# Optimization experiments

Hardware: AMD Instinct MI355X
Metric: run time of the kernel (lower is better)

## Reference

```python
import jax, jax.numpy as jnp
import numpy as np

H = 4          # num_heads
D = 32         # out_dim per head (P, A, state all 32)
NP_ = 30000    # number of P nodes
NA_ = 30000    # number of A nodes
NS_ = 1        # single global state node
E = 400000     # edges per agent-agent edge type
ALPHA = 0.2    # leaky-relu negative slope


def _edge_type(Wh_et, Wh_dst, a_src, a_dst, src, dst, n_dst):
    """GAT attention + edge-softmax + scatter-aggregate for one edge type.
    Wh_et: [N_src,H,D] edge-type projected src features; Wh_dst: [N_dst,H,D]."""
    es = jnp.sum(Wh_et * a_src, axis=-1)    # [N_src,H]
    ed = jnp.sum(Wh_dst * a_dst, axis=-1)   # [N_dst,H]
    e = es[src] + ed[dst]                   # [E,H] u_add_v
    e = jnp.where(e > 0, e, ALPHA * e)      # leaky relu
    m = jax.ops.segment_max(e, dst, num_segments=n_dst)
    m = jnp.where(jnp.isfinite(m), m, 0.0)  # guard empty segments
    w = jnp.exp(e - m[dst])                 # [E,H]
    denom = jax.ops.segment_sum(w, dst, num_segments=n_dst)
    a = w / denom[dst]                      # edge softmax over dst neighborhoods
    msg = Wh_et[src] * a[:, :, None]        # [E,H,D] u_mul_e
    return jax.ops.segment_sum(msg, dst, num_segments=n_dst)  # fn.sum


def setup_inputs() -> dict:
    key = jax.random.key(0)
    ks = iter(jax.random.split(key, 64))
    nrm = lambda shape, s=0.05: jax.random.normal(next(ks), shape, jnp.float32) * s
    inp = {}
    inp['feat_P'] = nrm((NP_, 128), 1.0)
    inp['feat_A'] = nrm((NA_, 128), 1.0)
    inp['feat_state'] = nrm((NS_, 64), 1.0)
    for name, din in [('P', 128), ('A', 128), ('p2p', 128), ('p2a', 128),
                      ('a2p', 128), ('a2a', 128), ('p2s', 128), ('a2s', 128), ('in', 64)]:
        inp['W_' + name] = nrm((din, H * D))
        inp['b_' + name] = nrm((H * D,))
    for et in ['p2p', 'p2a', 'a2p', 'a2a', 'p2s', 'a2s']:
        inp['attn_%s_src' % et] = nrm((H, D))
        inp['attn_%s_dst' % et] = nrm((H, D))
    ri = lambda n, hi: jax.random.randint(next(ks), (n,), 0, hi, jnp.int32)
    inp['src_p2p'] = ri(E, NP_); inp['dst_p2p'] = ri(E, NP_)
    inp['src_p2a'] = ri(E, NP_); inp['dst_p2a'] = ri(E, NA_)
    inp['src_a2p'] = ri(E, NA_); inp['dst_a2p'] = ri(E, NP_)
    inp['src_a2a'] = ri(E, NA_); inp['dst_a2a'] = ri(E, NA_)
    inp['src_p2s'] = jnp.arange(NP_, dtype=jnp.int32); inp['dst_p2s'] = jnp.zeros((NP_,), jnp.int32)
    inp['src_a2s'] = jnp.arange(NA_, dtype=jnp.int32); inp['dst_a2s'] = jnp.zeros((NA_,), jnp.int32)
    return inp


def reference(feat_P, feat_A, feat_state,
              W_P, b_P, W_A, b_A, W_p2p, b_p2p, W_p2a, b_p2a, W_a2p, b_a2p,
              W_a2a, b_a2a, W_p2s, b_p2s, W_a2s, b_a2s, W_in, b_in,
              attn_p2p_src, attn_p2p_dst, attn_p2a_src, attn_p2a_dst,
              attn_a2p_src, attn_a2p_dst, attn_a2a_src, attn_a2a_dst,
              attn_p2s_src, attn_p2s_dst, attn_a2s_src, attn_a2s_dst,
              src_p2p, dst_p2p, src_p2a, dst_p2a, src_a2p, dst_a2p,
              src_a2a, dst_a2a, src_p2s, dst_p2s, src_a2s, dst_a2s):
    lin = lambda x, W, b: (x @ W + b).reshape(-1, H, D)
    # self transforms
    Wh_P = lin(feat_P, W_P, b_P)
    Wh_A = lin(feat_A, W_A, b_A)
    Wh_in = lin(feat_state, W_in, b_in)
    # per-edge-type transforms
    Wh_p2p = lin(feat_P, W_p2p, b_p2p)
    Wh_p2a = lin(feat_P, W_p2a, b_p2a)
    Wh_a2p = lin(feat_A, W_a2p, b_a2p)
    Wh_a2a = lin(feat_A, W_a2a, b_a2a)
    Wh_p2s = lin(feat_P, W_p2s, b_p2s)
    Wh_a2s = lin(feat_A, W_a2s, b_a2s)
    # attention + edge softmax + aggregate per edge type
    ft_p2p = _edge_type(Wh_p2p, Wh_P, attn_p2p_src, attn_p2p_dst, src_p2p, dst_p2p, NP_)
    ft_a2p = _edge_type(Wh_a2p, Wh_P, attn_a2p_src, attn_a2p_dst, src_a2p, dst_a2p, NP_)
    ft_p2a = _edge_type(Wh_p2a, Wh_A, attn_p2a_src, attn_p2a_dst, src_p2a, dst_p2a, NA_)
    ft_a2a = _edge_type(Wh_a2a, Wh_A, attn_a2a_src, attn_a2a_dst, src_a2a, dst_a2a, NA_)
    ft_p2s = _edge_type(Wh_p2s, Wh_in, attn_p2s_src, attn_p2s_dst, src_p2s, dst_p2s, NS_)
    ft_a2s = _edge_type(Wh_a2s, Wh_in, attn_a2s_src, attn_a2s_dst, src_a2s, dst_a2s, NS_)
    out_P = jax.nn.relu(Wh_P + ft_p2p + ft_a2p)      # [NP,H,D]
    out_A = jax.nn.relu(Wh_A + ft_p2a + ft_a2a)      # [NA,H,D]
    out_S = jax.nn.relu(Wh_in + ft_p2s + ft_a2s)     # [1,H,D]
    # concat along node axis (all out dims are D) for a single output tensor
    return jnp.concatenate([out_P, out_A, out_S], axis=0)
```

## Files before the change

### kernel.cpp

```cpp
#include <hip/hip_runtime.h>

#define NP 30000
#define NA 30000
#define EDG 400000
#define HD 128
#define LRELU_ALPHA 0.2f
#define NODE_STRIDE 30016
#define TILE 32
#define BPJ 938

__device__ __forceinline__ float lrelu(float x) { return x > 0.f ? x : LRELU_ALPHA * x; }

struct GJob {
    const float* A; const float* W; const float* bias;
    float* C;
    const float* a1; float* o1;
    const float* a2; float* o2;
    int mode;
};
struct GJobs { GJob j[4]; };

__launch_bounds__(256)
__global__ void gemm_multi(GJobs js)
{
    const GJob J = js.j[blockIdx.y];
    __shared__ float As[TILE * 128];
    __shared__ float red[4][128];
    __shared__ float dred[4][4];
    const int t = threadIdx.x;
    const int row0 = blockIdx.x * TILE;
    const int M = NP;
    #pragma unroll
    for (int i = 0; i < 4; ++i) {
        int f4 = t + i * 256;
        int r = f4 >> 5, c4 = f4 & 31;
        int gr = row0 + r;
        float4 v = make_float4(0.f, 0.f, 0.f, 0.f);
        if (gr < M) v = reinterpret_cast<const float4*>(J.A)[(size_t)gr * 32 + c4];
        reinterpret_cast<float4*>(As)[f4] = v;
    }
    __syncthreads();
    const int cg = t & 63;
    const int rg = t >> 6;
    float acc0[8], acc1[8];
    #pragma unroll
    for (int r = 0; r < 8; ++r) { acc0[r] = 0.f; acc1[r] = 0.f; }
    const float* Asr = &As[rg * 8 * 128];
    const float* W = J.W;
    for (int k = 0; k < 128; k += 4) {
        float w00 = W[(k+0)*128 + cg],    w01 = W[(k+1)*128 + cg],
              w02 = W[(k+2)*128 + cg],    w03 = W[(k+3)*128 + cg];
        float w10 = W[(k+0)*128 + cg+64], w11 = W[(k+1)*128 + cg+64],
              w12 = W[(k+2)*128 + cg+64], w13 = W[(k+3)*128 + cg+64];
        #pragma unroll
        for (int r = 0; r < 8; ++r) {
            float4 f = *reinterpret_cast<const float4*>(&Asr[r * 128 + k]);
            acc0[r] += f.x*w00 + f.y*w01 + f.z*w02 + f.w*w03;
            acc1[r] += f.x*w10 + f.y*w11 + f.z*w12 + f.w*w13;
        }
    }
    float b0 = J.bias[cg], b1 = J.bias[cg + 64];
    #pragma unroll
    for (int r = 0; r < 8; ++r) { acc0[r] += b0; acc1[r] += b1; }

    if (J.mode != 2) {
        #pragma unroll
        for (int r = 0; r < 8; ++r) {
            int gr = row0 + rg * 8 + r;
            if (gr < M) {
                J.C[(size_t)gr * 128 + cg]      = acc0[r];
                J.C[(size_t)gr * 128 + cg + 64] = acc1[r];
            }
        }
        const int nrd = (J.mode == 0) ? 2 : 1;
        float a10 = J.a1[cg], a11 = J.a1[cg + 64];
        float a20 = 0.f, a21 = 0.f;
        if (nrd == 2) { a20 = J.a2[cg]; a21 = J.a2[cg + 64]; }
        #pragma unroll
        for (int r = 0; r < 8; ++r) {
            int node = row0 + rg * 8 + r;
            if (node >= M) break;
            float t10 = acc0[r] * a10, t11 = acc1[r] * a11;
            float t20 = acc0[r] * a20, t21 = acc1[r] * a21;
            #pragma unroll
            for (int off = 16; off; off >>= 1) {
                t10 += __shfl_xor(t10, off, 32);
                t11 += __shfl_xor(t11, off, 32);
                t20 += __shfl_xor(t20, off, 32);
                t21 += __shfl_xor(t21, off, 32);
            }
            if (cg == 0)  { J.o1[node*4+0] = t10; J.o1[node*4+2] = t11;
                            if (nrd == 2) { J.o2[node*4+0] = t20; J.o2[node*4+2] = t21; } }
            if (cg == 32) { J.o1[node*4+1] = t10; J.o1[node*4+3] = t11;
                            if (nrd == 2) { J.o2[node*4+1] = t20; J.o2[node*4+3] = t21; } }
        }
    } else {
        float av0 = J.a1[cg], av1 = J.a1[cg + 64];
        float e0 = J.a2[cg >> 5];
        float e1 = J.a2[2 + (cg >> 5)];
        float sacc0 = 0.f, sacc1 = 0.f, ds0 = 0.f, ds1 = 0.f;
        #pragma unroll
        for (int r = 0; r < 8; ++r) {
            int node = row0 + rg * 8 + r;
            if (node >= M) break;
            float f0 = acc0[r], f1 = acc1[r];
            float t0 = f0 * av0, t1 = f1 * av1;
            #pragma unroll
            for (int off = 16; off; off >>= 1) {
                t0 += __shfl_xor(t0, off, 32);
                t1 += __shfl_xor(t1, off, 32);
            }
            float w0 = __expf(lrelu(t0 + e0));
            float w1 = __expf(lrelu(t1 + e1));
            sacc0 += w0 * f0; sacc1 += w1 * f1;
            ds0 += w0; ds1 += w1;
        }
        red[rg][cg] = sacc0;
        red[rg][cg + 64] = sacc1;
        if (cg == 0)  { dred[rg][0] = ds0; dred[rg][2] = ds1; }
        if (cg == 32) { dred[rg][1] = ds0; dred[rg][3] = ds1; }
        __syncthreads();
        if (t < 128) {
            float s = red[0][t] + red[1][t] + red[2][t] + red[3][t];
            atomicAdd(&J.o1[t], s);
        }
        if (t < 4) {
            float s = dred[0][t] + dred[1][t] + dred[2][t] + dred[3][t];
            atomicAdd(&J.o2[t], s);
        }
    }
}

__global__ void state_lin(const float* __restrict__ feat, const float* __restrict__ W,
                          const float* __restrict__ b, float* __restrict__ out, int K)
{
    int n = threadIdx.x;
    float acc = b[n];
    for (int k = 0; k < K; ++k) acc += feat[k] * W[k * 128 + n];
    out[n] = acc;
}

__global__ void edot2(const float* __restrict__ Wh_inb, const float* __restrict__ aP,
                      const float* __restrict__ aA, float* __restrict__ edsP,
                      float* __restrict__ edsA)
{
    int t = threadIdx.x;
    int l = t & 31;
    float v = Wh_inb[t];
    float p = v * aP[t];
    float q = v * aA[t];
    #pragma unroll
    for (int off = 16; off; off >>= 1) {
        p += __shfl_xor(p, off, 32);
        q += __shfl_xor(q, off, 32);
    }
    if (l == 0) { edsP[t >> 5] = p; edsA[t >> 5] = q; }
}

struct EdgeJobs { const int* src[4]; const int* dst[4]; int* srcsOut[4]; };

__launch_bounds__(256)
__global__ void hist4(EdgeJobs ej, int* __restrict__ counts)
{
    int y = blockIdx.y;
    int e = blockIdx.x * 256 + threadIdx.x;
    if (e < EDG) atomicAdd(&counts[y * NODE_STRIDE + ej.dst[y][e]], 1);
}

__launch_bounds__(1024)
__global__ void scan4(const int* __restrict__ counts, int* __restrict__ offsets,
                      int* __restrict__ cursor, int n)
{
    const int* cnt = counts + blockIdx.x * NODE_STRIDE;
    int* off = offsets + blockIdx.x * NODE_STRIDE;
    int* cur = cursor + blockIdx.x * NODE_STRIDE;
    int t = threadIdx.x;
    int lane = t & 63, wv = t >> 6;
    __shared__ int wsum[16];
    __shared__ int carry_s;
    if (t == 0) { carry_s = 0; off[0] = 0; }
    __syncthreads();
    for (int base = 0; base < n; base += 1024) {
        int i = base + t;
        int v = (i < n) ? cnt[i] : 0;
        int x = v;
        #pragma unroll
        for (int o = 1; o < 64; o <<= 1) {
            int y = __shfl_up(x, o, 64);
            if (lane >= o) x += y;
        }
        if (lane == 63) wsum[wv] = x;
        __syncthreads();
        if (wv == 0) {
            int y = (lane < 16) ? wsum[lane] : 0;
            #pragma unroll
            for (int o = 1; o < 16; o <<= 1) {
                int z = __shfl_up(y, o, 64);
                if (lane >= o) y += z;
            }
            if (lane < 16) wsum[lane] = y;
        }
        __syncthreads();
        int add = carry_s + (wv > 0 ? wsum[wv - 1] : 0);
        int incl = x + add;
        if (i < n) { off[i + 1] = incl; cur[i] = incl - v; }
        __syncthreads();
        if (t == 0) carry_s += wsum[15];
        __syncthreads();
    }
}

__launch_bounds__(256)
__global__ void scatter4(EdgeJobs ej, int* __restrict__ cursor)
{
    int y = blockIdx.y;
    int e = blockIdx.x * 256 + threadIdx.x;
    if (e >= EDG) return;
    int d = ej.dst[y][e];
    int pos = atomicAdd(&cursor[y * NODE_STRIDE + d], 1);
    ej.srcsOut[y][pos] = ej.src[y][e];
}

__launch_bounds__(256)
__global__ void aggregate2(const float* __restrict__ Wh0, const int* __restrict__ off0,
                           const int* __restrict__ srcs0, const float* __restrict__ es0,
                           const float* __restrict__ ed0,
                           const float* __restrict__ Wh1, const int* __restrict__ off1,
                           const int* __restrict__ srcs1, const float* __restrict__ es1,
                           const float* __restrict__ ed1,
                           float* __restrict__ out, int n)
{
    int lane = threadIdx.x & 63;
    int node = (blockIdx.x * blockDim.x + threadIdx.x) >> 6;
    if (node >= n) return;
    const int h = lane >> 4;
    float accX0 = 0.f, accY0 = 0.f, d0 = 0.f;
    float accX1 = 0.f, accY1 = 0.f, d1 = 0.f;
    {
        float edv = ed0[node * 4 + h];
        int b = off0[node], e = off0[node + 1];
        int i = b;
        for (; i + 4 <= e; i += 4) {
            int s0 = srcs0[i], s1 = srcs0[i+1], s2 = srcs0[i+2], s3 = srcs0[i+3];
            float w0 = __expf(lrelu(es0[s0*4 + h] + edv));
            float w1 = __expf(lrelu(es0[s1*4 + h] + edv));
            float w2 = __expf(lrelu(es0[s2*4 + h] + edv));
            float w3 = __expf(lrelu(es0[s3*4 + h] + edv));
            float2 x0 = *reinterpret_cast<const float2*>(&Wh0[(size_t)s0*128 + lane*2]);
            float2 x1 = *reinterpret_cast<const float2*>(&Wh0[(size_t)s1*128 + lane*2]);
            float2 x2 = *reinterpret_cast<const float2*>(&Wh0[(size_t)s2*128 + lane*2]);
            float2 x3 = *reinterpret_cast<const float2*>(&Wh0[(size_t)s3*128 + lane*2]);
            accX0 += w0*x0.x + w1*x1.x + w2*x2.x + w3*x3.x;
            accY0 += w0*x0.y + w1*x1.y + w2*x2.y + w3*x3.y;
            d0 += w0 + w1 + w2 + w3;
        }
        for (; i < e; ++i) {
            int s = srcs0[i];
            float w = __expf(lrelu(es0[s*4 + h] + edv));
            float2 x = *reinterpret_cast<const float2*>(&Wh0[(size_t)s*128 + lane*2]);
            accX0 += w * x.x; accY0 += w * x.y; d0 += w;
        }
    }
    {
        float edv = ed1[node * 4 + h];
        int b = off1[node], e = off1[node + 1];
        int i = b;
        for (; i + 4 <= e; i += 4) {
            int s0 = srcs1[i], s1 = srcs1[i+1], s2 = srcs1[i+2], s3 = srcs1[i+3];
            float w0 = __expf(lrelu(es1[s0*4 + h] + edv));
            float w1 = __expf(lrelu(es1[s1*4 + h] + edv));
            float w2 = __expf(lrelu(es1[s2*4 + h] + edv));
            float w3 = __expf(lrelu(es1[s3*4 + h] + edv));
            float2 x0 = *reinterpret_cast<const float2*>(&Wh1[(size_t)s0*128 + lane*2]);
            float2 x1 = *reinterpret_cast<const float2*>(&Wh1[(size_t)s1*128 + lane*2]);
            float2 x2 = *reinterpret_cast<const float2*>(&Wh1[(size_t)s2*128 + lane*2]);
            float2 x3 = *reinterpret_cast<const float2*>(&Wh1[(size_t)s3*128 + lane*2]);
            accX1 += w0*x0.x + w1*x1.x + w2*x2.x + w3*x3.x;
            accY1 += w0*x0.y + w1*x1.y + w2*x2.y + w3*x3.y;
            d1 += w0 + w1 + w2 + w3;
        }
        for (; i < e; ++i) {
            int s = srcs1[i];
            float w = __expf(lrelu(es1[s*4 + h] + edv));
            float2 x = *reinterpret_cast<const float2*>(&Wh1[(size_t)s*128 + lane*2]);
            accX1 += w * x.x; accY1 += w * x.y; d1 += w;
        }
    }
    float i0 = d0 > 0.f ? 1.f / d0 : 0.f;
    float i1 = d1 > 0.f ? 1.f / d1 : 0.f;
    float2* op = reinterpret_cast<float2*>(out + (size_t)node * 128) + lane;
    float2 o = *op;
    o.x += accX0 * i0 + accX1 * i1;
    o.y += accY0 * i0 + accY1 * i1;
    o.x = o.x > 0.f ? o.x : 0.f;
    o.y = o.y > 0.f ? o.y : 0.f;
    *op = o;
}

__global__ void finalize_state(const float* __restrict__ Wh_in, const float* __restrict__ SS0,
                               const float* __restrict__ dS0, const float* __restrict__ SS1,
                               const float* __restrict__ dS1, float* __restrict__ out)
{
    int t = threadIdx.x;
    int h = t >> 5;
    float v0 = dS0[h]; float i0 = v0 > 0.f ? 1.f / v0 : 0.f;
    float v1 = dS1[h]; float i1 = v1 > 0.f ? 1.f / v1 : 0.f;
    float v = Wh_in[t] + SS0[t] * i0 + SS1[t] * i1;
    out[t] = v > 0.f ? v : 0.f;
}

extern "C" void kernel_launch(void* const* d_in, const int* in_sizes, int n_in,
                              void* d_out, int out_size, void* d_ws, size_t ws_size,
                              hipStream_t stream)
{
    const float* feat_P = (const float*)d_in[0];
    const float* feat_A = (const float*)d_in[1];
    const float* feat_state = (const float*)d_in[2];
    const float* W_P   = (const float*)d_in[3];  const float* b_P   = (const float*)d_in[4];
    const float* W_A   = (const float*)d_in[5];  const float* b_A   = (const float*)d_in[6];
    const float* W_p2p = (const float*)d_in[7];  const float* b_p2p = (const float*)d_in[8];
    const float* W_p2a = (const float*)d_in[9];  const float* b_p2a = (const float*)d_in[10];
    const float* W_a2p = (const float*)d_in[11]; const float* b_a2p = (const float*)d_in[12];
    const float* W_a2a = (const float*)d_in[13]; const float* b_a2a = (const float*)d_in[14];
    const float* W_p2s = (const float*)d_in[15]; const float* b_p2s = (const float*)d_in[16];
    const float* W_a2s = (const float*)d_in[17]; const float* b_a2s = (const float*)d_in[18];
    const float* W_in  = (const float*)d_in[19]; const float* b_in  = (const float*)d_in[20];
    const float* at_p2p_s = (const float*)d_in[21]; const float* at_p2p_d = (const float*)d_in[22];
    const float* at_p2a_s = (const float*)d_in[23]; const float* at_p2a_d = (const float*)d_in[24];
    const float* at_a2p_s = (const float*)d_in[25]; const float* at_a2p_d = (const float*)d_in[26];
    const float* at_a2a_s = (const float*)d_in[27]; const float* at_a2a_d = (const float*)d_in[28];
    const float* at_p2s_s = (const float*)d_in[29]; const float* at_p2s_d = (const float*)d_in[30];
    const float* at_a2s_s = (const float*)d_in[31]; const float* at_a2s_d = (const float*)d_in[32];
    const int* src_p2p = (const int*)d_in[33]; const int* dst_p2p = (const int*)d_in[34];
    const int* src_p2a = (const int*)d_in[35]; const int* dst_p2a = (const int*)d_in[36];
    const int* src_a2p = (const int*)d_in[37]; const int* dst_a2p = (const int*)d_in[38];
    const int* src_a2a = (const int*)d_in[39]; const int* dst_a2a = (const int*)d_in[40];
    float* out = (float*)d_out;

    char* base = (char*)d_ws;
    float* WhT0   = (float*)base;  base += (size_t)NP * HD * 4;
    float* WhT1   = (float*)base;  base += (size_t)NP * HD * 4;
    int* srcs_p2p = (int*)base;    base += (size_t)EDG * 4;
    int* srcs_a2p = (int*)base;    base += (size_t)EDG * 4;
    int* srcs_p2a = (int*)base;    base += (size_t)EDG * 4;
    int* srcs_a2a = (int*)base;    base += (size_t)EDG * 4;
    float* es_p2p = (float*)base;  base += NP * 4 * 4;
    float* es_a2p = (float*)base;  base += NA * 4 * 4;
    float* es_p2a = (float*)base;  base += NP * 4 * 4;
    float* es_a2a = (float*)base;  base += NA * 4 * 4;
    float* ed_p2p = (float*)base;  base += NP * 4 * 4;
    float* ed_a2p = (float*)base;  base += NP * 4 * 4;
    float* ed_p2a = (float*)base;  base += NA * 4 * 4;
    float* ed_a2a = (float*)base;  base += NA * 4 * 4;
    int*   counts = (int*)base;    base += 4 * NODE_STRIDE * 4;
    int*   cursor = (int*)base;    base += 4 * NODE_STRIDE * 4;
    int*   offs   = (int*)base;    base += 4 * NODE_STRIDE * 4;
    float* Wh_inb = (float*)base;  base += 128 * 4;
    float* SS0    = (float*)base;  base += 128 * 4;
    float* SS1    = (float*)base;  base += 128 * 4;
    float* dS0    = (float*)base;  base += 4 * 4;
    float* dS1    = (float*)base;  base += 4 * 4;
    float* edsP   = (float*)base;  base += 4 * 4;
    float* edsA   = (float*)base;  base += 4 * 4;
    size_t needed = (size_t)(base - (char*)d_ws);
    if (ws_size < needed) return;

    int* off_p2p = offs;
    int* off_a2p = offs + NODE_STRIDE;
    int* off_p2a = offs + 2 * NODE_STRIDE;
    int* off_a2a = offs + 3 * NODE_STRIDE;

    float* outP = out;
    float* outA = out + (size_t)NP * HD;
    float* outS = out + (size_t)(NP + NA) * HD;

    const dim3 B(256);
    const int gNodeW64 = (NP * 64 + 255) / 256;
    const int gEdgeT = (EDG + 255) / 256;

    EdgeJobs ej;
    ej.src[0] = src_p2p; ej.dst[0] = dst_p2p; ej.srcsOut[0] = srcs_p2p;
    ej.src[1] = src_a2p; ej.dst[1] = dst_a2p; ej.srcsOut[1] = srcs_a2p;
    ej.src[2] = src_p2a; ej.dst[2] = dst_p2a; ej.srcsOut[2] = srcs_p2a;
    ej.src[3] = src_a2a; ej.dst[3] = dst_a2a; ej.srcsOut[3] = srcs_a2a;
    hipMemsetAsync(counts, 0, 4 * NODE_STRIDE * sizeof(int), stream);
    hist4<<<dim3(gEdgeT, 4), B, 0, stream>>>(ej, counts);
    scan4<<<4, 1024, 0, stream>>>(counts, offs, cursor, NP);
    scatter4<<<dim3(gEdgeT, 4), B, 0, stream>>>(ej, cursor);

    hipMemsetAsync(SS0, 0, (128 + 128 + 4 + 4) * sizeof(float), stream);
    state_lin<<<1, 128, 0, stream>>>(feat_state, W_in, b_in, Wh_inb, 64);
    edot2<<<1, 128, 0, stream>>>(Wh_inb, at_p2s_d, at_a2s_d, edsP, edsA);

    {
        GJobs g;
        g.j[0] = { feat_P, W_P,   b_P,   outP, at_p2p_d, ed_p2p, at_a2p_d, ed_a2p, 0 };
        g.j[1] = { feat_A, W_A,   b_A,   outA, at_p2a_d, ed_p2a, at_a2a_d, ed_a2a, 0 };
        g.j[2] = { feat_P, W_p2p, b_p2p, WhT0, at_p2p_s, es_p2p, nullptr,  nullptr, 1 };
        g.j[3] = { feat_A, W_a2p, b_a2p, WhT1, at_a2p_s, es_a2p, nullptr,  nullptr, 1 };
        gemm_multi<<<dim3(BPJ, 4), B, 0, stream>>>(g);
    }
    aggregate2<<<gNodeW64, B, 0, stream>>>(WhT0, off_p2p, srcs_p2p, es_p2p, ed_p2p,
                                           WhT1, off_a2p, srcs_a2p, es_a2p, ed_a2p,
                                           outP, NP);

    {
        GJobs g;
        g.j[0] = { feat_P, W_p2a, b_p2a, WhT0,    at_p2a_s, es_p2a, nullptr, nullptr, 1 };
        g.j[1] = { feat_A, W_a2a, b_a2a, WhT1,    at_a2a_s, es_a2a, nullptr, nullptr, 1 };
        g.j[2] = { feat_P, W_p2s, b_p2s, nullptr, at_p2s_s, SS0,    edsP,    dS0,     2 };
        g.j[3] = { feat_A, W_a2s, b_a2s, nullptr, at_a2s_s, SS1,    edsA,    dS1,     2 };
        gemm_multi<<<dim3(BPJ, 4), B, 0, stream>>>(g);
    }
    aggregate2<<<gNodeW64, B, 0, stream>>>(WhT0, off_p2a, srcs_p2a, es_p2a, ed_p2a,
                                           WhT1, off_a2a, srcs_a2a, es_a2a, ed_a2a,
                                           outA, NA);

    finalize_state<<<1, 128, 0, stream>>>(Wh_inb, SS0, dS0, SS1, dS1, outS);
}
```

Baseline: 742.7 us.

## Compute edge-type projections with bf16 MFMA and gather bf16 features in aggregation

Adds a bf16 MFMA GEMM kernel that computes all four edge-type source projections in one launch. It stores them as bf16 and writes the per-head source attention scores from the fp32 accumulators. The aggregation kernels now gather half-width bf16 rows, which halves the random-gather traffic. The remaining fp32 GEMM launch handles the dst projections and state terms, and the schedule is regrouped so both aggregations run after the GEMMs. The cost is bf16 rounding of inputs, weights and stored features, which adds numerical error against the fp32 reference.

Measured after the change: 636.5 us. -14.3%, faster.

```diff
diff --git a/kernel.cpp b/kernel.cpp
--- a/kernel.cpp
+++ b/kernel.cpp
@@ -8,8 +8,119 @@
 #define NODE_STRIDE 30016
 #define TILE 32
 #define BPJ 938
+#define MTILE 64
+#define MBPJ 469
+#define WS_OFF 16384
+
+typedef __attribute__((ext_vector_type(8))) short short8;
+typedef __attribute__((ext_vector_type(4))) float f32x4;
 
 __device__ __forceinline__ float lrelu(float x) { return x > 0.f ? x : LRELU_ALPHA * x; }
+
+__device__ __forceinline__ unsigned short f2bf(float f) {
+    unsigned u = __float_as_uint(f);
+    u += 0x7fffu + ((u >> 16) & 1u);
+    return (unsigned short)(u >> 16);
+}
+
+struct MJob {
+    const float* A; const float* W; const float* bias;
+    unsigned short* C; const float* a1; float* es;
+};
+struct MJobs { MJob j[4]; };
+
+__launch_bounds__(256)
+__global__ void gemm_mfma(MJobs js)
+{
+    const MJob J = js.j[blockIdx.y];
+    __shared__ alignas(16) char lds[49152];
+    const int t = threadIdx.x;
+    const int row0 = blockIdx.x * MTILE;
+    const int M = NP;
+
+    #pragma unroll
+    for (int i = 0; i < 4; ++i) {
+        int c = t + i * 256;
+        int row = c >> 4, k0 = (c & 15) * 8;
+        int gr = row0 + row;
+        float4 v0 = make_float4(0.f,0.f,0.f,0.f), v1 = v0;
+        if (gr < M) {
+            v0 = reinterpret_cast<const float4*>(J.A)[(size_t)gr * 32 + (k0 >> 2)];
+            v1 = reinterpret_cast<const float4*>(J.A)[(size_t)gr * 32 + (k0 >> 2) + 1];
+        }
+        short8 p;
+        p[0]=f2bf(v0.x); p[1]=f2bf(v0.y); p[2]=f2bf(v0.z); p[3]=f2bf(v0.w);
+        p[4]=f2bf(v1.x); p[5]=f2bf(v1.y); p[6]=f2bf(v1.z); p[7]=f2bf(v1.w);
+        int byte = (row * 256 + k0 * 2) ^ ((row & 7) << 4);
+        *reinterpret_cast<short8*>(lds + byte) = p;
+    }
+    {
+        int c4 = (t & 31) * 4;
+        int kk = (t >> 5) * 16;
+        unsigned short wb[4][16];
+        #pragma unroll
+        for (int k = 0; k < 16; ++k) {
+            float4 v = reinterpret_cast<const float4*>(J.W)[(kk + k) * 32 + (c4 >> 2)];
+            wb[0][k]=f2bf(v.x); wb[1][k]=f2bf(v.y); wb[2][k]=f2bf(v.z); wb[3][k]=f2bf(v.w);
+        }
+        #pragma unroll
+        for (int j = 0; j < 4; ++j) {
+            int col = c4 + j;
+            short8 s0, s1;
+            #pragma unroll
+            for (int q = 0; q < 8; ++q) { s0[q] = (short)wb[j][q]; s1[q] = (short)wb[j][q+8]; }
+            int inner = col * 256 + kk * 2;
+            int x = (col & 7) << 4;
+            *reinterpret_cast<short8*>(lds + WS_OFF + ((inner)      ^ x)) = s0;
+            *reinterpret_cast<short8*>(lds + WS_OFF + ((inner + 16) ^ x)) = s1;
+        }
+    }
+    __syncthreads();
+
+    const int l = t & 63, w = t >> 6;
+    f32x4 acc[8];
+    #pragma unroll
+    for (int ct = 0; ct < 8; ++ct) {
+        float bv = J.bias[ct * 16 + (l & 15)];
+        acc[ct] = (f32x4){bv, bv, bv, bv};
+    }
+    const int arow = w * 16 + (l & 15);
+    const int abase = arow * 256 + ((l >> 4) * 16);
+    const int axor = (arow & 7) << 4;
+    const int bxor = ((l & 15) & 7) << 4;
+    #pragma unroll
+    for (int kc = 0; kc < 4; ++kc) {
+        short8 af = *reinterpret_cast<const short8*>(lds + ((abase + kc * 64) ^ axor));
+        #pragma unroll
+        for (int ct = 0; ct < 8; ++ct) {
+            int binner = (ct * 16 + (l & 15)) * 256 + kc * 64 + ((l >> 4) * 16);
+            short8 bf8 = *reinterpret_cast<const short8*>(lds + WS_OFF + (binner ^ bxor));
+            acc[ct] = __builtin_amdgcn_mfma_f32_16x16x32_bf16(af, bf8, acc[ct], 0, 0, 0);
+        }
+    }
+    #pragma unroll
+    for (int r = 0; r < 4; ++r) {
+        int grow = row0 + w * 16 + (l >> 4) * 4 + r;
+        if (grow < M) {
+            #pragma unroll
+            for (int ct = 0; ct < 8; ++ct)
+                J.C[(size_t)grow * 128 + ct * 16 + (l & 15)] = f2bf(acc[ct][r]);
+        }
+    }
+    #pragma unroll
+    for (int h = 0; h < 4; ++h) {
+        float alo = J.a1[h * 32 + (l & 15)];
+        float ahi = J.a1[h * 32 + 16 + (l & 15)];
+        #pragma unroll
+        for (int r = 0; r < 4; ++r) {
+            float p = acc[2*h][r] * alo + acc[2*h+1][r] * ahi;
+            p += __shfl_xor(p, 1); p += __shfl_xor(p, 2);
+            p += __shfl_xor(p, 4); p += __shfl_xor(p, 8);
+            int grow = row0 + w * 16 + (l >> 4) * 4 + r;
+            if ((l & 15) == 0 && grow < M) J.es[grow * 4 + h] = p;
+        }
+    }
+}
 
 struct GJob {
     const float* A; const float* W; const float* bias;
@@ -72,10 +183,8 @@
                 J.C[(size_t)gr * 128 + cg + 64] = acc1[r];
             }
         }
-        const int nrd = (J.mode == 0) ? 2 : 1;
         float a10 = J.a1[cg], a11 = J.a1[cg + 64];
-        float a20 = 0.f, a21 = 0.f;
-        if (nrd == 2) { a20 = J.a2[cg]; a21 = J.a2[cg + 64]; }
+        float a20 = J.a2[cg], a21 = J.a2[cg + 64];
         #pragma unroll
         for (int r = 0; r < 8; ++r) {
             int node = row0 + rg * 8 + r;
@@ -90,9 +199,9 @@
                 t21 += __shfl_xor(t21, off, 32);
             }
             if (cg == 0)  { J.o1[node*4+0] = t10; J.o1[node*4+2] = t11;
-                            if (nrd == 2) { J.o2[node*4+0] = t20; J.o2[node*4+2] = t21; } }
+                            J.o2[node*4+0] = t20; J.o2[node*4+2] = t21; }
             if (cg == 32) { J.o1[node*4+1] = t10; J.o1[node*4+3] = t11;
-                            if (nrd == 2) { J.o2[node*4+1] = t20; J.o2[node*4+3] = t21; } }
+                            J.o2[node*4+1] = t20; J.o2[node*4+3] = t21; }
         }
     } else {
         float av0 = J.a1[cg], av1 = J.a1[cg + 64];
@@ -222,10 +331,10 @@
 }
 
 __launch_bounds__(256)
-__global__ void aggregate2(const float* __restrict__ Wh0, const int* __restrict__ off0,
+__global__ void aggregate2(const unsigned* __restrict__ Wh0, const int* __restrict__ off0,
                            const int* __restrict__ srcs0, const float* __restrict__ es0,
                            const float* __restrict__ ed0,
-                           const float* __restrict__ Wh1, const int* __restrict__ off1,
+                           const unsigned* __restrict__ Wh1, const int* __restrict__ off1,
                            const int* __restrict__ srcs1, const float* __restrict__ es1,
                            const float* __restrict__ ed1,
                            float* __restrict__ out, int n)
@@ -246,19 +355,23 @@
             float w1 = __expf(lrelu(es0[s1*4 + h] + edv));
             float w2 = __expf(lrelu(es0[s2*4 + h] + edv));
             float w3 = __expf(lrelu(es0[s3*4 + h] + edv));
-            float2 x0 = *reinterpret_cast<const float2*>(&Wh0[(size_t)s0*128 + lane*2]);
-            float2 x1 = *reinterpret_cast<const float2*>(&Wh0[(size_t)s1*128 + lane*2]);
-            float2 x2 = *reinterpret_cast<const float2*>(&Wh0[(size_t)s2*128 + lane*2]);
-            float2 x3 = *reinterpret_cast<const float2*>(&Wh0[(size_t)s3*128 + lane*2]);
-            accX0 += w0*x0.x + w1*x1.x + w2*x2.x + w3*x3.x;
-            accY0 += w0*x0.y + w1*x1.y + w2*x2.y + w3*x3.y;
+            unsigned x0 = Wh0[(size_t)s0*64 + lane];
+            unsigned x1 = Wh0[(size_t)s1*64 + lane];
+            unsigned x2 = Wh0[(size_t)s2*64 + lane];
+            unsigned x3 = Wh0[(size_t)s3*64 + lane];
+            accX0 += w0*__uint_as_float(x0<<16) + w1*__uint_as_float(x1<<16)
+                   + w2*__uint_as_float(x2<<16) + w3*__uint_as_float(x3<<16);
+            accY0 += w0*__uint_as_float(x0&0xffff0000u) + w1*__uint_as_float(x1&0xffff0000u)
+                   + w2*__uint_as_float(x2&0xffff0000u) + w3*__uint_as_float(x3&0xffff0000u);
             d0 += w0 + w1 + w2 + w3;
         }
         for (; i < e; ++i) {
             int s = srcs0[i];
             float w = __expf(lrelu(es0[s*4 + h] + edv));
-            float2 x = *reinterpret_cast<const float2*>(&Wh0[(size_t)s*128 + lane*2]);
-            accX0 += w * x.x; accY0 += w * x.y; d0 += w;
+            unsigned x = Wh0[(size_t)s*64 + lane];
+            accX0 += w * __uint_as_float(x<<16);
+            accY0 += w * __uint_as_float(x&0xffff0000u);
+            d0 += w;
         }
     }
     {
@@ -271,19 +384,23 @@
             float w1 = __expf(lrelu(es1[s1*4 + h] + edv));
             float w2 = __expf(lrelu(es1[s2*4 + h] + edv));
             float w3 = __expf(lrelu(es1[s3*4 + h] + edv));
-            float2 x0 = *reinterpret_cast<const float2*>(&Wh1[(size_t)s0*128 + lane*2]);
-            float2 x1 = *reinterpret_cast<const float2*>(&Wh1[(size_t)s1*128 + lane*2]);
-            float2 x2 = *reinterpret_cast<const float2*>(&Wh1[(size_t)s2*128 + lane*2]);
-            float2 x3 = *reinterpret_cast<const float2*>(&Wh1[(size_t)s3*128 + lane*2]);
-            accX1 += w0*x0.x + w1*x1.x + w2*x2.x + w3*x3.x;
-            accY1 += w0*x0.y + w1*x1.y + w2*x2.y + w3*x3.y;
+            unsigned x0 = Wh1[(size_t)s0*64 + lane];
+            unsigned x1 = Wh1[(size_t)s1*64 + lane];
+            unsigned x2 = Wh1[(size_t)s2*64 + lane];
+            unsigned x3 = Wh1[(size_t)s3*64 + lane];
+            accX1 += w0*__uint_as_float(x0<<16) + w1*__uint_as_float(x1<<16)
+                   + w2*__uint_as_float(x2<<16) + w3*__uint_as_float(x3<<16);
+            accY1 += w0*__uint_as_float(x0&0xffff0000u) + w1*__uint_as_float(x1&0xffff0000u)
+                   + w2*__uint_as_float(x2&0xffff0000u) + w3*__uint_as_float(x3&0xffff0000u);
             d1 += w0 + w1 + w2 + w3;
         }
         for (; i < e; ++i) {
             int s = srcs1[i];
             float w = __expf(lrelu(es1[s*4 + h] + edv));
-            float2 x = *reinterpret_cast<const float2*>(&Wh1[(size_t)s*128 + lane*2]);
-            accX1 += w * x.x; accY1 += w * x.y; d1 += w;
+            unsigned x = Wh1[(size_t)s*64 + lane];
+            accX1 += w * __uint_as_float(x<<16);
+            accY1 += w * __uint_as_float(x&0xffff0000u);
+            d1 += w;
         }
     }
     float i0 = d0 > 0.f ? 1.f / d0 : 0.f;
@@ -338,8 +455,10 @@
     float* out = (float*)d_out;
 
     char* base = (char*)d_ws;
-    float* WhT0   = (float*)base;  base += (size_t)NP * HD * 4;
-    float* WhT1   = (float*)base;  base += (size_t)NP * HD * 4;
+    unsigned short* bT_p2p = (unsigned short*)base; base += (size_t)NP * HD * 2;
+    unsigned short* bT_a2p = (unsigned short*)base; base += (size_t)NA * HD * 2;
+    unsigned short* bT_p2a = (unsigned short*)base; base += (size_t)NP * HD * 2;
+    unsigned short* bT_a2a = (unsigned short*)base; base += (size_t)NA * HD * 2;
     int* srcs_p2p = (int*)base;    base += (size_t)EDG * 4;
     int* srcs_a2p = (int*)base;    base += (size_t)EDG * 4;
     int* srcs_p2a = (int*)base;    base += (size_t)EDG * 4;
@@ -393,27 +512,27 @@
     edot2<<<1, 128, 0, stream>>>(Wh_inb, at_p2s_d, at_a2s_d, edsP, edsA);
 
     {
-        GJobs g;
-        g.j[0] = { feat_P, W_P,   b_P,   outP, at_p2p_d, ed_p2p, at_a2p_d, ed_a2p, 0 };
-        g.j[1] = { feat_A, W_A,   b_A,   outA, at_p2a_d, ed_p2a, at_a2a_d, ed_a2a, 0 };
-        g.j[2] = { feat_P, W_p2p, b_p2p, WhT0, at_p2p_s, es_p2p, nullptr,  nullptr, 1 };
-        g.j[3] = { feat_A, W_a2p, b_a2p, WhT1, at_a2p_s, es_a2p, nullptr,  nullptr, 1 };
-        gemm_multi<<<dim3(BPJ, 4), B, 0, stream>>>(g);
-    }
-    aggregate2<<<gNodeW64, B, 0, stream>>>(WhT0, off_p2p, srcs_p2p, es_p2p, ed_p2p,
-                                           WhT1, off_a2p, srcs_a2p, es_a2p, ed_a2p,
-                                           outP, NP);
-
+        MJobs m;
+        m.j[0] = { feat_P, W_p2p, b_p2p, bT_p2p, at_p2p_s, es_p2p };
+        m.j[1] = { feat_A, W_a2p, b_a2p, bT_a2p, at_a2p_s, es_a2p };
+        m.j[2] = { feat_P, W_p2a, b_p2a, bT_p2a, at_p2a_s, es_p2a };
+        m.j[3] = { feat_A, W_a2a, b_a2a, bT_a2a, at_a2a_s, es_a2a };
+        gemm_mfma<<<dim3(MBPJ, 4), B, 0, stream>>>(m);
+    }
     {
         GJobs g;
-        g.j[0] = { feat_P, W_p2a, b_p2a, WhT0,    at_p2a_s, es_p2a, nullptr, nullptr, 1 };
-        g.j[1] = { feat_A, W_a2a, b_a2a, WhT1,    at_a2a_s, es_a2a, nullptr, nullptr, 1 };
-        g.j[2] = { feat_P, W_p2s, b_p2s, nullptr, at_p2s_s, SS0,    edsP,    dS0,     2 };
-        g.j[3] = { feat_A, W_a2s, b_a2s, nullptr, at_a2s_s, SS1,    edsA,    dS1,     2 };
+        g.j[0] = { feat_P, W_P,   b_P,   outP,    at_p2p_d, ed_p2p, at_a2p_d, ed_a2p, 0 };
+        g.j[1] = { feat_A, W_A,   b_A,   outA,    at_p2a_d, ed_p2a, at_a2a_d, ed_a2a, 0 };
+        g.j[2] = { feat_P, W_p2s, b_p2s, nullptr, at_p2s_s, SS0,    edsP,     dS0,    2 };
+        g.j[3] = { feat_A, W_a2s, b_a2s, nullptr, at_a2s_s, SS1,    edsA,     dS1,    2 };
         gemm_multi<<<dim3(BPJ, 4), B, 0, stream>>>(g);
     }
-    aggregate2<<<gNodeW64, B, 0, stream>>>(WhT0, off_p2a, srcs_p2a, es_p2a, ed_p2a,
-                                           WhT1, off_a2a, srcs_a2a, es_a2a, ed_a2a,
+
+    aggregate2<<<gNodeW64, B, 0, stream>>>((const unsigned*)bT_p2p, off_p2p, srcs_p2p, es_p2p, ed_p2p,
+                                           (const unsigned*)bT_a2p, off_a2p, srcs_a2p, es_a2p, ed_a2p,
+                                           outP, NP);
+    aggregate2<<<gNodeW64, B, 0, stream>>>((const unsigned*)bT_p2a, off_p2a, srcs_p2a, es_p2a, ed_p2a,
+                                           (const unsigned*)bT_a2a, off_a2a, srcs_a2a, es_a2a, ed_a2a,
                                            outA, NA);
 
     finalize_state<<<1, 128, 0, stream>>>(Wh_inb, SS0, dS0, SS1, dS1, outS);
```
